# Optimization experiments

Measured on AMD Instinct MI355X. Metric: run time of the kernel, lower is better.

## Reference

```python
import jax, jax.numpy as jnp
import numpy as np

B, T, D, H, O = 256, 512, 256, 1024, 256


def _uniform(key, shape, fan_in):
    # kaiming_uniform with a=0.1: bound = sqrt(6 / ((1 + a^2) * fan_in))
    bound = float(np.sqrt(6.0 / ((1.0 + 0.1 ** 2) * fan_in)))
    return jax.random.uniform(key, shape, jnp.float32, -bound, bound)


def setup_inputs() -> dict:
    key = jax.random.key(0)
    ks = jax.random.split(key, 8)
    inp = {
        "x": jax.random.normal(ks[0], (B, T, D), jnp.float32),
        "W_gx": _uniform(ks[1], (D, H), D),
        "W_gh": _uniform(ks[2], (H, H), H),
        "b_g": jnp.zeros((H,), jnp.float32),
        "W_ix": _uniform(ks[3], (D, H), D),
        "W_ih": _uniform(ks[4], (H, H), H),
        "b_i": jnp.zeros((H,), jnp.float32),
        "W_fx": _uniform(ks[5], (D, H), D),
        "W_fh": _uniform(ks[6], (H, H), H),
        "b_f": jnp.zeros((H,), jnp.float32),
        "W_ox": _uniform(jax.random.fold_in(key, 10), (D, H), D),
        "W_oh": _uniform(jax.random.fold_in(key, 11), (H, H), H),
        "b_o": jnp.zeros((H,), jnp.float32),
        "W_ph": _uniform(ks[7], (H, O), H),
        "b_p": jnp.zeros((O,), jnp.float32),
    }
    return inp


def reference(x, W_gx, W_gh, b_g, W_ix, W_ih, b_i, W_fx, W_fh, b_f,
              W_ox, W_oh, b_o, W_ph, b_p):
    Hd = W_gh.shape[0]
    # Fuse the 4 per-gate matmuls into two GEMMs (same math as the loop).
    Wx = jnp.concatenate([W_gx, W_ix, W_fx, W_ox], axis=1)  # [D, 4H]
    Wh = jnp.concatenate([W_gh, W_ih, W_fh, W_oh], axis=1)  # [H, 4H]
    b = jnp.concatenate([b_g, b_i, b_f, b_o])               # [4H]
    xW = jnp.einsum('btd,dk->tbk', x, Wx) + b                # [T, B, 4H]

    def step(carry, xw_t):
        h, c = carry
        z = xw_t + h @ Wh                                    # [B, 4H]
        g = jnp.tanh(z[:, :Hd])
        i = jax.nn.sigmoid(z[:, Hd:2 * Hd])
        f = jax.nn.sigmoid(z[:, 2 * Hd:3 * Hd])
        o = jax.nn.sigmoid(z[:, 3 * Hd:])
        c = g * i + c * f
        h = jnp.tanh(c) * o
        return (h, c), None

    h0 = jnp.zeros((x.shape[0], Hd), x.dtype)
    (h, _), _ = jax.lax.scan(step, (h0, h0), xW)
    return jax.nn.softmax(h @ W_ph + b_p, axis=1)
```

## Files before the change

kernel.cpp:

```cpp
#include <hip/hip_runtime.h>


typedef _Float16 f16;
typedef _Float16 f16x8 __attribute__((ext_vector_type(8)));
typedef _Float16 f16x4 __attribute__((ext_vector_type(4)));
typedef float f32x4 __attribute__((ext_vector_type(4)));
typedef unsigned int u32;

#define WS_WT    0
#define WS_WPHT  10485760
#define WS_HBUF  11010048
#define WS_LG    12058624
#define WS_CNT   12320768
#define WS_TICK  12322816

#define ZBASE 81920u
#define ZKH   12288u
#define ZGATE 3072u
#define ZROW  192u
#define CBUF  131072u
#define BCAST 135168

__device__ __forceinline__ float sigm(float v) { return 1.0f / (1.0f + __expf(-v)); }
__device__ __forceinline__ float tanhfast(float v) {
  float t = __expf(-2.0f * fabsf(v));
  float r = (1.0f - t) / (1.0f + t);
  return v < 0.0f ? -r : r;
}

__global__ __launch_bounds__(256) void prep_wt(
    const float* __restrict__ Wgh, const float* __restrict__ Wih,
    const float* __restrict__ Wfh, const float* __restrict__ Woh,
    const float* __restrict__ Wgx, const float* __restrict__ Wix,
    const float* __restrict__ Wfx, const float* __restrict__ Wox,
    f16* __restrict__ WT)
{
  __shared__ float tile[32][33];
  int bid = blockIdx.x;
  int gate = bid / 1280;
  int rem  = bid % 1280;
  int jt = rem / 40, kt = rem % 40;
  const float* srcH = (gate==0)?Wgh:(gate==1)?Wih:(gate==2)?Wfh:Woh;
  const float* srcX = (gate==0)?Wgx:(gate==1)?Wix:(gate==2)?Wfx:Wox;
  const float* src = (kt < 32) ? (srcH + (size_t)(kt*32)*1024)
                               : (srcX + (size_t)(kt*32 - 1024)*1024);
  int t = threadIdx.x;
  {
    int jl = t & 31, kg = t >> 5;
#pragma unroll
    for (int it = 0; it < 4; ++it) {
      int kl = kg + it*8;
      tile[kl][jl] = src[(size_t)kl*1024 + jt*32 + jl];
    }
  }
  __syncthreads();
  {
    int kl = t & 31, jg = t >> 5;
#pragma unroll
    for (int it = 0; it < 4; ++it) {
      int jl2 = jg + it*8;
      WT[(size_t)(gate*1024 + jt*32 + jl2)*1280 + kt*32 + kl] = (f16)tile[kl][jl2];
    }
  }
}

__global__ __launch_bounds__(256) void prep_wph(const float* __restrict__ Wph,
                                                f16* __restrict__ WphT)
{
  __shared__ float tile[32][33];
  int bid = blockIdx.x;
  int jt = bid & 7, kt = bid >> 3;
  int t = threadIdx.x;
  {
    int jl = t & 31, kg = t >> 5;
#pragma unroll
    for (int it = 0; it < 4; ++it) {
      int kl = kg + it*8;
      tile[kl][jl] = Wph[(size_t)(kt*32 + kl)*256 + jt*32 + jl];
    }
  }
  __syncthreads();
  {
    int kl = t & 31, jg = t >> 5;
#pragma unroll
    for (int it = 0; it < 4; ++it) {
      int jl2 = jg + it*8;
      WphT[(size_t)(jt*32 + jl2)*1024 + kt*32 + kl] = (f16)tile[kl][jl2];
    }
  }
}

__global__ __launch_bounds__(512, 2) void lstm_main(
    const float* __restrict__ x, const f16* __restrict__ WT,
    const f16* __restrict__ WphT, f16* __restrict__ hbuf,
    const float* __restrict__ bgp, const float* __restrict__ bip,
    const float* __restrict__ bfp, const float* __restrict__ bop,
    const float* __restrict__ bpp, float* __restrict__ lg,
    u32* __restrict__ cnt, u32* __restrict__ tick, float* __restrict__ out)
{
  __shared__ __align__(16) char smem[135184];
  const int tid  = threadIdx.x;
  const int lane = tid & 63;
  const int wv   = tid >> 6;
  const int gate = wv & 3;
  const int kh   = wv >> 2;
  const int l15 = lane & 15, l4 = lane >> 4;

  u32 myxcd;
  asm volatile("s_getreg_b32 %0, hwreg(HW_REG_XCC_ID)" : "=s"(myxcd));
  myxcd &= 7u;
  if (tid == 0) {
    u32 t = __hip_atomic_fetch_add(tick + myxcd, 1u,
                                   __ATOMIC_RELAXED, __HIP_MEMORY_SCOPE_AGENT);
    *(volatile u32*)(smem + BCAST) = t;
  }
  if (wv == 0) {
    u32 v = 0;
    int guard = 0;
    for (;;) {
      v = (lane < 8) ? __hip_atomic_load(tick + lane, __ATOMIC_RELAXED,
                                         __HIP_MEMORY_SCOPE_AGENT) : 0u;
      u32 sum = v;
      sum += __shfl_xor(sum, 1);
      sum += __shfl_xor(sum, 2);
      sum += __shfl_xor(sum, 4);
      if (__shfl(sum, 0) == 256u) break;
      __builtin_amdgcn_s_sleep(1);
      if (++guard > (1 << 20)) break;
    }
    int even = __all((lane < 8) ? (v == 32u) : 1);
    if (lane == 0) *(volatile u32*)(smem + BCAST + 4) = (u32)even;
  }
  __syncthreads();
  const bool xloc = (*(volatile u32*)(smem + BCAST + 4)) != 0u;
  const u32 myticket = *(volatile u32*)(smem + BCAST);
  const int xg = xloc ? (int)myxcd    : (blockIdx.x & 7);
  const int cg = xloc ? (int)myticket : (blockIdx.x >> 3);
  u32* flg = cnt + xg*64;

  f16x8 Breg[20][2];
  {
    const f16* wb0 = WT + (size_t)(gate*1024 + cg*32 + l15)*1280 + kh*640 + l4*8;
    const f16* wb1 = wb0 + (size_t)16*1280;
#pragma unroll
    for (int kk = 0; kk < 20; ++kk) {
      Breg[kk][0] = *(const f16x8*)(wb0 + kk*32);
      asm volatile("" : "+v"(Breg[kk][0]));
      Breg[kk][1] = *(const f16x8*)(wb1 + kk*32);
      asm volatile("" : "+v"(Breg[kk][1]));
    }
  }

  const int bcol = cg*32 + (tid & 31);
  const float bgr = bgp[bcol], bir = bip[bcol], bfr = bfp[bcol], bor = bop[bcol];

  const u32 aoff = (u32)l15*2560u + (u32)(kh*1280 + l4*16);
  const u32 aswz = (u32)l15 << 4;
  const int srow = tid >> 5;
  const int sseg = tid & 31;
  const u32 swzr = (u32)srow << 4;

  *(float*)(smem + CBUF + tid*4) = 0.0f;
  *(float*)(smem + CBUF + 2048 + tid*4) = 0.0f;
  __syncthreads();

  u32 pre = 0xFFFFFFFFu;
  bool preOK = false;

#pragma unroll 1
  for (int slot = 0; slot < 1024; ++slot) {
    const int T = slot & 1, s = slot >> 1;
    const u32 Abase = (u32)T * 40960u;
    u32* flgT = flg + T*32;
    const int grow = xg*32 + T*16 + srow;

    {
      const float* xsrc = x + ((size_t)grow*512 + (size_t)s)*256;
      float4 xv0 = *(const float4*)(xsrc + (sseg     )*4);
      float4 xv1 = *(const float4*)(xsrc + (sseg + 32)*4);
      f16x4 hv;
      hv[0] = (f16)xv0.x; hv[1] = (f16)xv0.y; hv[2] = (f16)xv0.z; hv[3] = (f16)xv0.w;
      *(f16x4*)(smem + Abase + ((srow*2560u + 2048u + 8u*(u32)(sseg     )) ^ swzr)) = hv;
      hv[0] = (f16)xv1.x; hv[1] = (f16)xv1.y; hv[2] = (f16)xv1.z; hv[3] = (f16)xv1.w;
      *(f16x4*)(smem + Abase + ((srow*2560u + 2048u + 8u*(u32)(sseg + 32)) ^ swzr)) = hv;
    }
    if (s > 0) {
      if (wv == 0) {
        if (!preOK) {
          const u32 tgt = (u32)s;
          u32 v = tgt;
          int guard = 0;
          for (;;) {
            if (lane < 32)
              v = __hip_atomic_load(flgT + lane, __ATOMIC_RELAXED,
                                    __HIP_MEMORY_SCOPE_AGENT);
            if (__all(v >= tgt)) break;
            __builtin_amdgcn_s_sleep(1);
            if (++guard > (1 << 18)) break;
          }
        }
        if (lane == 0) {
          if (xloc) {
            asm volatile("buffer_inv sc0\n\ts_waitcnt vmcnt(0)" ::: "memory");
          } else {
            __threadfence();
          }
        }
      }
    }
    __syncthreads();
    {
      const f16* hsrc = hbuf + (size_t)(s & 1)*262144 + (size_t)grow*1024;
#pragma unroll
      for (int j = 0; j < 4; ++j) {
        int chunk = sseg + 32*j;
        uint4 v = *(const uint4*)(hsrc + chunk*8);
        *(uint4*)(smem + Abase + ((srow*2560u + 16u*(u32)chunk) ^ swzr)) = v;
      }
    }
    __syncthreads();
    {
      const int nT = (slot + 1) & 1, nS = (slot + 1) >> 1;
      pre = 0xFFFFFFFFu;
      if (wv == 0 && nS > 0 && nS < 512 && lane < 32)
        pre = __hip_atomic_load(flg + nT*32 + lane, __ATOMIC_RELAXED,
                                __HIP_MEMORY_SCOPE_AGENT);
    }
    f32x4 acc0 = {}, acc1 = {};
#pragma unroll
    for (int kk = 0; kk < 20; ++kk) {
      f16x8 av = *(const f16x8*)(smem + Abase + ((aoff + (u32)kk*64u) ^ aswz));
      acc0 = __builtin_amdgcn_mfma_f32_16x16x32_f16(av, Breg[kk][0], acc0, 0, 0, 0);
      acc1 = __builtin_amdgcn_mfma_f32_16x16x32_f16(av, Breg[kk][1], acc1, 0, 0, 0);
    }
    {
      const u32 zb = ZBASE + (u32)T*24576u + (u32)kh*ZKH + (u32)gate*ZGATE
                   + (u32)l15*4u;
#pragma unroll
      for (int i = 0; i < 4; ++i) {
        u32 r0 = (u32)(l4*4 + i);
        *(float*)(smem + zb + r0*ZROW)       = acc0[i];
        *(float*)(smem + zb + r0*ZROW + 64u) = acc1[i];
      }
    }
    __syncthreads();
    {
      f16* hw = hbuf + (size_t)((s & 1) ^ 1)*262144;
      const int row = tid >> 5, col = tid & 31;
      const int gcol = cg*32 + col;
      const u32 zo = ZBASE + (u32)T*24576u + (u32)row*ZROW + (u32)col*4u;
      float zg = *(const float*)(smem + zo + 0u*ZGATE)
               + *(const float*)(smem + zo + 0u*ZGATE + ZKH) + bgr;
      float zi = *(const float*)(smem + zo + 1u*ZGATE)
               + *(const float*)(smem + zo + 1u*ZGATE + ZKH) + bir;
      float zf = *(const float*)(smem + zo + 2u*ZGATE)
               + *(const float*)(smem + zo + 2u*ZGATE + ZKH) + bfr;
      float zv = *(const float*)(smem + zo + 3u*ZGATE)
               + *(const float*)(smem + zo + 3u*ZGATE + ZKH) + bor;
      float* cp = (float*)(smem + CBUF + (u32)T*2048u + (u32)(row*32 + col)*4u);
      float cv = *cp;
      float gv = tanhfast(zg);
      float iv = sigm(zi);
      float fv = sigm(zf);
      float ov = sigm(zv);
      float cn = gv*iv + cv*fv;
      *cp = cn;
      hw[(size_t)(xg*32 + T*16 + row)*1024 + gcol] = (f16)(tanhfast(cn) * ov);
    }
    __syncthreads();
    if (tid == 0) {
      if (!xloc) __threadfence();
      __hip_atomic_store(flgT + cg, (u32)(s + 1),
                         __ATOMIC_RELAXED, __HIP_MEMORY_SCOPE_AGENT);
    }
    if (wv == 0) {
      const int nS = (slot + 1) >> 1;
      preOK = (nS == 0) || (nS >= 512) || __all(pre >= (u32)nS);
    }
  }

  if (wv == 0) {
    u32 v = 512u;
    int guard = 0;
    for (;;) {
      v = __hip_atomic_load(flg + lane, __ATOMIC_RELAXED,
                            __HIP_MEMORY_SCOPE_AGENT);
      if (__all(v >= 512u)) break;
      __builtin_amdgcn_s_sleep(1);
      if (++guard > (1 << 18)) break;
    }
    if (lane == 0) {
      if (xloc) { asm volatile("buffer_inv sc0\n\ts_waitcnt vmcnt(0)" ::: "memory"); }
      else      { __threadfence(); }
    }
  }
  __syncthreads();
  {
#pragma unroll 1
    for (int p = 0; p < 32; ++p) {
      int rowl = wv*4 + (p >> 3);
      int oc   = p & 7;
      const f16* hp = hbuf + (size_t)(xg*32 + rowl)*1024 + lane*16;
      const f16* wp = WphT + (size_t)(cg*8 + oc)*1024 + lane*16;
      f16x8 h0 = *(const f16x8*)hp;
      f16x8 h1 = *(const f16x8*)(hp + 8);
      f16x8 w0 = *(const f16x8*)wp;
      f16x8 w1 = *(const f16x8*)(wp + 8);
      float sum = 0.f;
#pragma unroll
      for (int q = 0; q < 8; ++q)
        sum += (float)h0[q]*(float)w0[q] + (float)h1[q]*(float)w1[q];
#pragma unroll
      for (int d = 1; d < 64; d <<= 1) sum += __shfl_xor(sum, d);
      if (lane == 0)
        lg[(size_t)(xg*32 + rowl)*256 + cg*8 + oc] = sum + bpp[cg*8 + oc];
    }
  }
  __syncthreads();
  if (tid == 0) {
    if (!xloc) __threadfence();
    __hip_atomic_store(flg + cg, 513u, __ATOMIC_RELAXED, __HIP_MEMORY_SCOPE_AGENT);
  }
  if (wv == 0) {
    u32 v = 513u;
    int guard = 0;
    for (;;) {
      if (lane < 32)
        v = __hip_atomic_load(flg + lane, __ATOMIC_RELAXED, __HIP_MEMORY_SCOPE_AGENT);
      if (__all(v >= 513u)) break;
      __builtin_amdgcn_s_sleep(1);
      if (++guard > (1 << 18)) break;
    }
    if (lane == 0) {
      if (xloc) { asm volatile("buffer_inv sc0\n\ts_waitcnt vmcnt(0)" ::: "memory"); }
      else      { __threadfence(); }
    }
  }
  __syncthreads();
  if (tid < 64) {
    int rowg = xg*32 + cg;
    const float* lr = lg + (size_t)rowg*256;
    float v0 = lr[tid], v1 = lr[tid+64], v2 = lr[tid+128], v3 = lr[tid+192];
    float mx = fmaxf(fmaxf(v0, v1), fmaxf(v2, v3));
#pragma unroll
    for (int d = 1; d < 64; d <<= 1) mx = fmaxf(mx, __shfl_xor(mx, d));
    float e0 = __expf(v0-mx), e1 = __expf(v1-mx), e2 = __expf(v2-mx), e3 = __expf(v3-mx);
    float sm = e0+e1+e2+e3;
#pragma unroll
    for (int d = 1; d < 64; d <<= 1) sm += __shfl_xor(sm, d);
    float inv = 1.0f / sm;
    float* orow = out + (size_t)rowg*256;
    orow[tid]      = e0*inv;
    orow[tid+64]   = e1*inv;
    orow[tid+128]  = e2*inv;
    orow[tid+192]  = e3*inv;
  }
}

extern "C" void kernel_launch(void* const* d_in, const int* in_sizes, int n_in,
                              void* d_out, int out_size, void* d_ws, size_t ws_size,
                              hipStream_t stream) {
  (void)in_sizes; (void)n_in; (void)out_size; (void)ws_size;
  const float* x   = (const float*)d_in[0];
  const float* Wgx = (const float*)d_in[1];
  const float* Wgh = (const float*)d_in[2];
  const float* bg  = (const float*)d_in[3];
  const float* Wix = (const float*)d_in[4];
  const float* Wih = (const float*)d_in[5];
  const float* bi  = (const float*)d_in[6];
  const float* Wfx = (const float*)d_in[7];
  const float* Wfh = (const float*)d_in[8];
  const float* bf  = (const float*)d_in[9];
  const float* Wox = (const float*)d_in[10];
  const float* Woh = (const float*)d_in[11];
  const float* bo  = (const float*)d_in[12];
  const float* Wph = (const float*)d_in[13];
  const float* bp  = (const float*)d_in[14];

  char* ws = (char*)d_ws;
  f16*   WT   = (f16*)(ws + WS_WT);
  f16*   WphT = (f16*)(ws + WS_WPHT);
  f16*   hbuf = (f16*)(ws + WS_HBUF);
  float* lg   = (float*)(ws + WS_LG);
  u32*   cnt  = (u32*)(ws + WS_CNT);
  u32*   tick = (u32*)(ws + WS_TICK);

  hipMemsetAsync(hbuf, 0, 524288, stream);
  hipMemsetAsync(cnt, 0, 2048 + 64, stream);

  prep_wt<<<5120, 256, 0, stream>>>(Wgh, Wih, Wfh, Woh, Wgx, Wix, Wfx, Wox, WT);
  prep_wph<<<256, 256, 0, stream>>>(Wph, WphT);
  lstm_main<<<256, 512, 0, stream>>>(x, WT, WphT, hbuf,
                                     bg, bi, bf, bo, bp,
                                     lg, cnt, tick, (float*)d_out);
}
```

Measured before the change: 2.505 ms.

## Interleave gates per lane and split K four ways to shrink gate exchange

New measurement: 2.485 ms. About the same (-0.8%).

```diff
diff --git a/kernel.cpp b/kernel.cpp
--- a/kernel.cpp
+++ b/kernel.cpp
@@ -14,12 +14,8 @@
 #define WS_CNT   12320768
 #define WS_TICK  12322816
 
-#define ZBASE 81920u
-#define ZKH   12288u
-#define ZGATE 3072u
-#define ZROW  192u
-#define CBUF  131072u
-#define BCAST 135168
+#define ZB    81920u
+#define BCAST 114688
 
 __device__ __forceinline__ float sigm(float v) { return 1.0f / (1.0f + __expf(-v)); }
 __device__ __forceinline__ float tanhfast(float v) {
@@ -98,12 +94,12 @@
     const float* __restrict__ bpp, float* __restrict__ lg,
     u32* __restrict__ cnt, u32* __restrict__ tick, float* __restrict__ out)
 {
-  __shared__ __align__(16) char smem[135184];
+  __shared__ __align__(16) char smem[114704];
   const int tid  = threadIdx.x;
   const int lane = tid & 63;
   const int wv   = tid >> 6;
-  const int gate = wv & 3;
-  const int kh   = wv >> 2;
+  const int hgrp = wv & 1;
+  const int kh   = wv >> 1;
   const int l15 = lane & 15, l4 = lane >> 4;
 
   u32 myxcd;
@@ -138,31 +134,31 @@
   const int cg = xloc ? (int)myticket : (blockIdx.x >> 3);
   u32* flg = cnt + xg*64;
 
-  f16x8 Breg[20][2];
-  {
-    const f16* wb0 = WT + (size_t)(gate*1024 + cg*32 + l15)*1280 + kh*640 + l4*8;
-    const f16* wb1 = wb0 + (size_t)16*1280;
-#pragma unroll
-    for (int kk = 0; kk < 20; ++kk) {
-      Breg[kk][0] = *(const f16x8*)(wb0 + kk*32);
-      asm volatile("" : "+v"(Breg[kk][0]));
-      Breg[kk][1] = *(const f16x8*)(wb1 + kk*32);
-      asm volatile("" : "+v"(Breg[kk][1]));
+  f16x8 Breg[10][4];
+  {
+    const int gate = l15 & 3, hsub = l15 >> 2;
+#pragma unroll
+    for (int f = 0; f < 4; ++f) {
+      const int n = gate*1024 + cg*32 + hgrp*16 + f*4 + hsub;
+      const f16* wb = WT + (size_t)n*1280 + kh*320 + l4*8;
+#pragma unroll
+      for (int kk = 0; kk < 10; ++kk) {
+        Breg[kk][f] = *(const f16x8*)(wb + kk*32);
+        asm volatile("" : "+v"(Breg[kk][f]));
+      }
     }
   }
 
   const int bcol = cg*32 + (tid & 31);
   const float bgr = bgp[bcol], bir = bip[bcol], bfr = bfp[bcol], bor = bop[bcol];
 
-  const u32 aoff = (u32)l15*2560u + (u32)(kh*1280 + l4*16);
+  const u32 aoff = (u32)l15*2560u + (u32)(kh*640 + l4*16);
   const u32 aswz = (u32)l15 << 4;
   const int srow = tid >> 5;
   const int sseg = tid & 31;
   const u32 swzr = (u32)srow << 4;
 
-  *(float*)(smem + CBUF + tid*4) = 0.0f;
-  *(float*)(smem + CBUF + 2048 + tid*4) = 0.0f;
-  __syncthreads();
+  float cA = 0.0f, cB = 0.0f;
 
   u32 pre = 0xFFFFFFFFu;
   bool preOK = false;
@@ -184,31 +180,23 @@
       hv[0] = (f16)xv1.x; hv[1] = (f16)xv1.y; hv[2] = (f16)xv1.z; hv[3] = (f16)xv1.w;
       *(f16x4*)(smem + Abase + ((srow*2560u + 2048u + 8u*(u32)(sseg + 32)) ^ swzr)) = hv;
     }
-    if (s > 0) {
-      if (wv == 0) {
-        if (!preOK) {
-          const u32 tgt = (u32)s;
-          u32 v = tgt;
-          int guard = 0;
-          for (;;) {
-            if (lane < 32)
-              v = __hip_atomic_load(flgT + lane, __ATOMIC_RELAXED,
-                                    __HIP_MEMORY_SCOPE_AGENT);
-            if (__all(v >= tgt)) break;
-            __builtin_amdgcn_s_sleep(1);
-            if (++guard > (1 << 18)) break;
-          }
-        }
-        if (lane == 0) {
-          if (xloc) {
-            asm volatile("buffer_inv sc0\n\ts_waitcnt vmcnt(0)" ::: "memory");
-          } else {
-            __threadfence();
-          }
-        }
-      }
-    }
-    __syncthreads();
+    if (s > 0 && !preOK) {
+      const u32 tgt = (u32)s;
+      u32 v = tgt;
+      int guard = 0;
+      for (;;) {
+        if (lane < 32)
+          v = __hip_atomic_load(flgT + lane, __ATOMIC_RELAXED,
+                                __HIP_MEMORY_SCOPE_AGENT);
+        if (__all(v >= tgt)) break;
+        __builtin_amdgcn_s_sleep(1);
+        if (++guard > (1 << 18)) break;
+      }
+      if (lane == 0) {
+        if (xloc) { asm volatile("buffer_inv sc0\n\ts_waitcnt vmcnt(0)" ::: "memory"); }
+        else      { __threadfence(); }
+      }
+    }
     {
       const f16* hsrc = hbuf + (size_t)(s & 1)*262144 + (size_t)grow*1024;
 #pragma unroll
@@ -219,63 +207,68 @@
       }
     }
     __syncthreads();
+    f32x4 acc0 = {}, acc1 = {}, acc2 = {}, acc3 = {};
+#pragma unroll
+    for (int kk = 0; kk < 10; ++kk) {
+      f16x8 av = *(const f16x8*)(smem + Abase + ((aoff + (u32)kk*64u) ^ aswz));
+      acc0 = __builtin_amdgcn_mfma_f32_16x16x32_f16(Breg[kk][0], av, acc0, 0, 0, 0);
+      acc1 = __builtin_amdgcn_mfma_f32_16x16x32_f16(Breg[kk][1], av, acc1, 0, 0, 0);
+      acc2 = __builtin_amdgcn_mfma_f32_16x16x32_f16(Breg[kk][2], av, acc2, 0, 0, 0);
+      acc3 = __builtin_amdgcn_mfma_f32_16x16x32_f16(Breg[kk][3], av, acc3, 0, 0, 0);
+    }
     {
       const int nT = (slot + 1) & 1, nS = (slot + 1) >> 1;
       pre = 0xFFFFFFFFu;
-      if (wv == 0 && nS > 0 && nS < 512 && lane < 32)
+      if (nS > 0 && nS < 512 && lane < 32)
         pre = __hip_atomic_load(flg + nT*32 + lane, __ATOMIC_RELAXED,
                                 __HIP_MEMORY_SCOPE_AGENT);
     }
-    f32x4 acc0 = {}, acc1 = {};
-#pragma unroll
-    for (int kk = 0; kk < 20; ++kk) {
-      f16x8 av = *(const f16x8*)(smem + Abase + ((aoff + (u32)kk*64u) ^ aswz));
-      acc0 = __builtin_amdgcn_mfma_f32_16x16x32_f16(av, Breg[kk][0], acc0, 0, 0, 0);
-      acc1 = __builtin_amdgcn_mfma_f32_16x16x32_f16(av, Breg[kk][1], acc1, 0, 0, 0);
-    }
-    {
-      const u32 zb = ZBASE + (u32)T*24576u + (u32)kh*ZKH + (u32)gate*ZGATE
-                   + (u32)l15*4u;
-#pragma unroll
-      for (int i = 0; i < 4; ++i) {
-        u32 r0 = (u32)(l4*4 + i);
-        *(float*)(smem + zb + r0*ZROW)       = acc0[i];
-        *(float*)(smem + zb + r0*ZROW + 64u) = acc1[i];
+    {
+      const u32 zkh = ZB + (u32)kh*8192u;
+#pragma unroll
+      for (int f = 0; f < 4; ++f) {
+        const u32 hcol = (u32)(hgrp*16 + f*4 + l4);
+        const u32 s16 = ((u32)(l15*32) + hcol) ^ ((u32)(l15 & 7));
+        f32x4 acc = (f==0)?acc0:(f==1)?acc1:(f==2)?acc2:acc3;
+        *(f32x4*)(smem + zkh + s16*16u) = acc;
       }
     }
     __syncthreads();
     {
       f16* hw = hbuf + (size_t)((s & 1) ^ 1)*262144;
-      const int row = tid >> 5, col = tid & 31;
-      const int gcol = cg*32 + col;
-      const u32 zo = ZBASE + (u32)T*24576u + (u32)row*ZROW + (u32)col*4u;
-      float zg = *(const float*)(smem + zo + 0u*ZGATE)
-               + *(const float*)(smem + zo + 0u*ZGATE + ZKH) + bgr;
-      float zi = *(const float*)(smem + zo + 1u*ZGATE)
-               + *(const float*)(smem + zo + 1u*ZGATE + ZKH) + bir;
-      float zf = *(const float*)(smem + zo + 2u*ZGATE)
-               + *(const float*)(smem + zo + 2u*ZGATE + ZKH) + bfr;
-      float zv = *(const float*)(smem + zo + 3u*ZGATE)
-               + *(const float*)(smem + zo + 3u*ZGATE + ZKH) + bor;
-      float* cp = (float*)(smem + CBUF + (u32)T*2048u + (u32)(row*32 + col)*4u);
-      float cv = *cp;
+      const int row = tid >> 5, hcol = tid & 31;
+      const u32 s16 = ((u32)(row*32) + (u32)hcol) ^ ((u32)(row & 7));
+      const u32 ro = s16*16u;
+      f32x4 z0 = *(const f32x4*)(smem + ZB +        ro);
+      f32x4 z1 = *(const f32x4*)(smem + ZB + 8192u  + ro);
+      f32x4 z2 = *(const f32x4*)(smem + ZB + 16384u + ro);
+      f32x4 z3 = *(const f32x4*)(smem + ZB + 24576u + ro);
+      float zg = z0[0] + z1[0] + z2[0] + z3[0] + bgr;
+      float zi = z0[1] + z1[1] + z2[1] + z3[1] + bir;
+      float zf = z0[2] + z1[2] + z2[2] + z3[2] + bfr;
+      float zo = z0[3] + z1[3] + z2[3] + z3[3] + bor;
+      float cv = T ? cB : cA;
       float gv = tanhfast(zg);
       float iv = sigm(zi);
       float fv = sigm(zf);
-      float ov = sigm(zv);
+      float ov = sigm(zo);
       float cn = gv*iv + cv*fv;
-      *cp = cn;
-      hw[(size_t)(xg*32 + T*16 + row)*1024 + gcol] = (f16)(tanhfast(cn) * ov);
+      if (T) cB = cn; else cA = cn;
+      hw[(size_t)(xg*32 + T*16 + row)*1024 + cg*32 + hcol] = (f16)(tanhfast(cn) * ov);
+    }
+    {
+      const int nS = (slot + 1) >> 1;
+      bool ok = (nS >= 512) || __all(pre >= (u32)nS);
+      preOK = xloc && ok;
+      if (preOK && nS < 512 && lane == 0) {
+        asm volatile("buffer_inv sc0\n\ts_waitcnt vmcnt(0)" ::: "memory");
+      }
     }
     __syncthreads();
     if (tid == 0) {
       if (!xloc) __threadfence();
       __hip_atomic_store(flgT + cg, (u32)(s + 1),
                          __ATOMIC_RELAXED, __HIP_MEMORY_SCOPE_AGENT);
-    }
-    if (wv == 0) {
-      const int nS = (slot + 1) >> 1;
-      preOK = (nS == 0) || (nS >= 512) || __all(pre >= (u32)nS);
     }
   }
 
```
